# Kernel tuning notes

Measured on AMD Instinct MI355X. Metric: run time of the kernel, lower is better.

## Reference

```python
import jax, jax.numpy as jnp
import numpy as np

N_NODES = 100000
N_EDGES = 600000
HIDDEN = 128


def setup_inputs() -> dict:
    key = jax.random.key(0)
    ks = jax.random.split(key, 5)
    x = jax.random.normal(ks[0], (N_NODES, HIDDEN), dtype=jnp.float32)
    edge_index = jax.random.randint(ks[1], (2, N_EDGES), 0, N_NODES, dtype=jnp.int64)
    edge_weight = jax.random.uniform(ks[2], (N_EDGES,), dtype=jnp.float32)
    # MLP params: Linear(2*H+1 -> H), ReLU, Linear(H -> 1)
    W1 = jax.random.normal(ks[3], (2 * HIDDEN + 1, HIDDEN), dtype=jnp.float32) * (1.0 / np.sqrt(2 * HIDDEN + 1))
    b1 = jnp.zeros((HIDDEN,), dtype=jnp.float32)
    W2 = jax.random.normal(ks[4], (HIDDEN, 1), dtype=jnp.float32) * (1.0 / np.sqrt(HIDDEN))
    b2 = jnp.zeros((1,), dtype=jnp.float32)
    return {"x": x, "edge_index": edge_index, "edge_weight": edge_weight,
            "W1": W1, "b1": b1, "W2": W2, "b2": b2}


def reference(x, edge_index, edge_weight, W1, b1, W2, b2):
    num_nodes = x.shape[0]
    src = edge_index[0]
    tgt = edge_index[1]
    h_src = x[src]                      # [E, H] gather
    h_tgt = x[tgt]                      # [E, H] gather
    w = edge_weight[:, None]            # [E, 1]
    concat = jnp.concatenate([h_src, h_tgt, w], axis=-1)   # [E, 2H+1]
    hidden = jax.nn.relu(concat @ W1 + b1)                 # [E, H]
    scores = (hidden @ W2 + b2)[:, 0]                      # [E]
    # NOTE: the original _softmax_edge's max-pass uses index_put_(accumulate=True)
    # on a -inf buffer, so every touched entry stays -inf and is then replaced by 0;
    # the net effect is NO max subtraction. Faithful math: plain exp / segment_sum.
    exp_scores = jnp.exp(scores)
    sum_exp = jax.ops.segment_sum(exp_scores, tgt, num_segments=num_nodes)
    sum_exp = jnp.maximum(sum_exp, 1e-12)
    alpha = exp_scores / sum_exp[tgt]                      # [E]
    out = jax.ops.segment_sum(alpha[:, None] * h_src, tgt, num_segments=num_nodes)
    return x + out
```

## Files before the change

### kernel.cpp

```cpp
#include <hip/hip_runtime.h>
#include <hip/hip_bf16.h>

#define N_NODES 100000
#define N_EDGES 600000
#define HID 128
#define SCAN_NB 391
#define GEMM_BLOCKS 1563
#define FILL_BLOCKS 586


typedef short bf16x8 __attribute__((ext_vector_type(8)));
typedef float f32x4  __attribute__((ext_vector_type(4)));

__device__ inline unsigned short f2bf(float v) {
    __hip_bfloat16 h = __float2bfloat16(v);
    return *(unsigned short*)&h;
}
__device__ inline float2 bfpair(unsigned int u) {
    float lo = __uint_as_float(u << 16);
    float hi = __uint_as_float(u & 0xffff0000u);
    return make_float2(lo, hi);
}
__device__ inline void lds_barrier() {
    asm volatile("s_waitcnt lgkmcnt(0)" ::: "memory");
    __builtin_amdgcn_s_barrier();
}

__global__ __launch_bounds__(256) void k_prep(const float* __restrict__ W1,
                                              unsigned short* __restrict__ Bh,
                                              int* __restrict__ deg)
{
    int idx = blockIdx.x * 256 + threadIdx.x;
    if (idx < N_NODES) deg[idx] = 0;
    if (idx < 32768) {
        int n = idx & 255;
        int k = idx >> 8;
        float v = (n < HID) ? W1[k * HID + n] : W1[(HID + k) * HID + (n - HID)];
        Bh[(k >> 5) * 8192 + n * 32 + (k & 31)] = f2bf(v);
    }
}

__global__ __launch_bounds__(256) void k_count(const int* __restrict__ ei,
                                               int* __restrict__ deg)
{
    int e = blockIdx.x * blockDim.x + threadIdx.x;
    if (e < N_EDGES) atomicAdd(&deg[ei[N_EDGES + e]], 1);
}

__global__ __launch_bounds__(256) void k_rowptr(const int* __restrict__ deg,
                                                int* __restrict__ rowptr,
                                                int* __restrict__ cursor)
{
    __shared__ int s[256];
    int t = threadIdx.x;
    int b = blockIdx.x;
    int lim = b * 256;

    int acc = 0;
    for (int i = t; i < lim; i += 256) acc += deg[i];
    s[t] = acc;
    __syncthreads();
    #pragma unroll
    for (int off = 128; off > 0; off >>= 1) {
        if (t < off) s[t] += s[t + off];
        __syncthreads();
    }
    int pb = s[0];
    __syncthreads();

    int idx = lim + t;
    int v = (idx < N_NODES) ? deg[idx] : 0;
    s[t] = v;
    __syncthreads();
    #pragma unroll
    for (int off = 1; off < 256; off <<= 1) {
        int u = (t >= off) ? s[t - off] : 0;
        __syncthreads();
        s[t] += u;
        __syncthreads();
    }
    if (idx < N_NODES) {
        int r = pb + s[t] - v;
        rowptr[idx] = r;
        cursor[idx] = r;
    }
    if (idx == 0) rowptr[N_NODES] = N_EDGES;
}

__global__ __launch_bounds__(256) void k_gemm_fill(const float* __restrict__ x,
                                                   const unsigned short* __restrict__ BhG,
                                                   unsigned short* __restrict__ zbuf,
                                                   unsigned short* __restrict__ y2buf,
                                                   const int* __restrict__ ei,
                                                   const float* __restrict__ ew,
                                                   int* __restrict__ cursor,
                                                   uint2* __restrict__ eprs)
{
    __shared__ unsigned short Ah[64 * 32];

    if (blockIdx.x < FILL_BLOCKS) {
        int fb = blockIdx.x;
        for (int e = fb * 256 + threadIdx.x; e < N_EDGES; e += FILL_BLOCKS * 256) {
            int tgt = ei[N_EDGES + e];
            int pos = atomicAdd(&cursor[tgt], 1);
            eprs[pos] = make_uint2((unsigned int)ei[e], __float_as_uint(ew[e]));
        }
        return;
    }

    const int tid  = threadIdx.x;
    const int bm   = (blockIdx.x - FILL_BLOCKS) * 64;
    const int wave = tid >> 6;
    const int lane = tid & 63;
    const int q    = lane >> 4;
    const int ln   = lane & 15;

    const int rowA = tid >> 3;
    const int rowB = rowA + 32;
    const int f4   = tid & 7;
    const int gmA  = bm + rowA;
    const int gmB  = bm + rowB;
    const bool okA = gmA < N_NODES;
    const bool okB = gmB < N_NODES;
    const float* pxA = &x[(size_t)gmA * HID + f4 * 4];
    const float* pxB = &x[(size_t)gmB * HID + f4 * 4];

    f32x4 acc[4][4] = {};

    float4 vA = make_float4(0.f,0.f,0.f,0.f), vB = vA;
    float4 vAn = vA, vBn = vA;
    if (okA) vA = *(const float4*)pxA;
    if (okB) vB = *(const float4*)pxB;

    for (int ks = 0; ks < 4; ++ks) {
        const int k0 = ks * 32;
        {
            float4 v = vA;
            unsigned int ph0 = (unsigned int)f2bf(v.x) | ((unsigned int)f2bf(v.y) << 16);
            unsigned int ph1 = (unsigned int)f2bf(v.z) | ((unsigned int)f2bf(v.w) << 16);
            *(uint2*)&Ah[rowA * 32 + f4 * 4] = make_uint2(ph0, ph1);
            if (okA) *(uint2*)&zbuf[(size_t)gmA * 256 + 128 + k0 + f4 * 4] = make_uint2(ph0, ph1);
        }
        {
            float4 v = vB;
            unsigned int ph0 = (unsigned int)f2bf(v.x) | ((unsigned int)f2bf(v.y) << 16);
            unsigned int ph1 = (unsigned int)f2bf(v.z) | ((unsigned int)f2bf(v.w) << 16);
            *(uint2*)&Ah[rowB * 32 + f4 * 4] = make_uint2(ph0, ph1);
            if (okB) *(uint2*)&zbuf[(size_t)gmB * 256 + 128 + k0 + f4 * 4] = make_uint2(ph0, ph1);
        }
        lds_barrier();

        if (ks < 3) {
            vAn = okA ? *(const float4*)(pxA + (ks + 1) * 32) : make_float4(0.f,0.f,0.f,0.f);
            vBn = okB ? *(const float4*)(pxB + (ks + 1) * 32) : make_float4(0.f,0.f,0.f,0.f);
        }

        bf16x8 ah[4], bh[4];
        #pragma unroll
        for (int mt = 0; mt < 4; ++mt) {
            ah[mt] = *(const bf16x8*)&Ah[(mt * 16 + ln) * 32 + q * 8];
        }
        #pragma unroll
        for (int nt = 0; nt < 4; ++nt) {
            bh[nt] = *(const bf16x8*)&BhG[ks * 8192 + (wave * 64 + nt * 16 + ln) * 32 + q * 8];
        }
        #pragma unroll
        for (int mt = 0; mt < 4; ++mt) {
            #pragma unroll
            for (int nt = 0; nt < 4; ++nt) {
                acc[mt][nt] = __builtin_amdgcn_mfma_f32_16x16x32_bf16(bh[nt], ah[mt], acc[mt][nt], 0, 0, 0);
            }
        }
        lds_barrier();
        vA = vAn; vB = vBn;
    }

    #pragma unroll
    for (int mt = 0; mt < 4; ++mt) {
        int node = bm + mt * 16 + ln;
        if (node < N_NODES) {
            #pragma unroll
            for (int nt = 0; nt < 4; ++nt) {
                int col0 = wave * 64 + nt * 16 + q * 4;
                unsigned int lo = (unsigned int)f2bf(acc[mt][nt][0]) | ((unsigned int)f2bf(acc[mt][nt][1]) << 16);
                unsigned int hi = (unsigned int)f2bf(acc[mt][nt][2]) | ((unsigned int)f2bf(acc[mt][nt][3]) << 16);
                if (col0 < 128) *(uint2*)&zbuf[(size_t)node * 256 + col0] = make_uint2(lo, hi);
                else            *(uint2*)&y2buf[(size_t)node * 128 + (col0 - 128)] = make_uint2(lo, hi);
            }
        }
    }
}

__global__ __launch_bounds__(256) void k_fused(const unsigned int* __restrict__ zu,
                                               const unsigned int* __restrict__ y2u,
                                               const int* __restrict__ rowptr,
                                               const uint2* __restrict__ eprs,
                                               const float* __restrict__ x,
                                               const float* __restrict__ W1,
                                               const float* __restrict__ b1,
                                               const float* __restrict__ W2,
                                               const float* __restrict__ b2,
                                               float* __restrict__ out)
{
    int n = (blockIdx.x * blockDim.x + threadIdx.x) >> 6;
    int lane = threadIdx.x & 63;
    if (n >= N_NODES) return;
    int ql = lane & 15;
    int qi = lane >> 4;
    int c0 = ql * 8;

    uint4 uy2 = *(const uint4*)&y2u[(size_t)n * 64 + ql * 4];
    float2 y2a = bfpair(uy2.x), y2b = bfpair(uy2.y), y2c = bfpair(uy2.z), y2d = bfpair(uy2.w);
    float4 bv0 = *(const float4*)&b1[c0];
    float4 bv1 = *(const float4*)&b1[c0 + 4];
    float4 wr0 = *(const float4*)&W1[256 * HID + c0];
    float4 wr1 = *(const float4*)&W1[256 * HID + c0 + 4];
    float4 w20 = *(const float4*)&W2[c0];
    float4 w21 = *(const float4*)&W2[c0 + 4];
    float p0 = y2a.x + bv0.x, p1 = y2a.y + bv0.y, p2 = y2b.x + bv0.z, p3 = y2b.y + bv0.w;
    float p4 = y2c.x + bv1.x, p5 = y2c.y + bv1.y, p6 = y2d.x + bv1.z, p7 = y2d.y + bv1.w;
    float b2v = b2[0];

    int beg = rowptr[n], end = rowptr[n + 1];
    float a0 = 0.f, a1 = 0.f, a2 = 0.f, a3 = 0.f;
    float a4 = 0.f, a5 = 0.f, a6 = 0.f, a7 = 0.f;
    float denom = 0.f;

    for (int i = beg; i < end; i += 4) {
        int idx = i + qi;
        bool valid = idx < end;
        int ie = valid ? idx : (end - 1);
        uint2 ep = eprs[ie];
        size_t base = (size_t)ep.x * 128;
        float w = __uint_as_float(ep.y);
        uint4 uy = *(const uint4*)&zu[base + ql * 4];
        uint4 ux = *(const uint4*)&zu[base + 64 + ql * 4];

        float2 ya = bfpair(uy.x), yb = bfpair(uy.y), yc = bfpair(uy.z), yd = bfpair(uy.w);
        float h0 = fmaxf(fmaf(w, wr0.x, ya.x + p0), 0.f);
        float h1 = fmaxf(fmaf(w, wr0.y, ya.y + p1), 0.f);
        float h2 = fmaxf(fmaf(w, wr0.z, yb.x + p2), 0.f);
        float h3 = fmaxf(fmaf(w, wr0.w, yb.y + p3), 0.f);
        float h4 = fmaxf(fmaf(w, wr1.x, yc.x + p4), 0.f);
        float h5 = fmaxf(fmaf(w, wr1.y, yc.y + p5), 0.f);
        float h6 = fmaxf(fmaf(w, wr1.z, yd.x + p6), 0.f);
        float h7 = fmaxf(fmaf(w, wr1.w, yd.y + p7), 0.f);
        float s = ((h0 * w20.x + h1 * w20.y) + (h2 * w20.z + h3 * w20.w))
                + ((h4 * w21.x + h5 * w21.y) + (h6 * w21.z + h7 * w21.w));
        #pragma unroll
        for (int m = 1; m <= 8; m <<= 1) s += __shfl_xor(s, m, 64);
        float es = valid ? __expf(s + b2v) : 0.f;

        float2 xa = bfpair(ux.x), xb = bfpair(ux.y), xc = bfpair(ux.z), xd = bfpair(ux.w);
        a0 = fmaf(es, xa.x, a0); a1 = fmaf(es, xa.y, a1);
        a2 = fmaf(es, xb.x, a2); a3 = fmaf(es, xb.y, a3);
        a4 = fmaf(es, xc.x, a4); a5 = fmaf(es, xc.y, a5);
        a6 = fmaf(es, xd.x, a6); a7 = fmaf(es, xd.y, a7);
        denom += es;
    }

    #pragma unroll
    for (int m = 16; m <= 32; m <<= 1) {
        a0 += __shfl_xor(a0, m, 64); a1 += __shfl_xor(a1, m, 64);
        a2 += __shfl_xor(a2, m, 64); a3 += __shfl_xor(a3, m, 64);
        a4 += __shfl_xor(a4, m, 64); a5 += __shfl_xor(a5, m, 64);
        a6 += __shfl_xor(a6, m, 64); a7 += __shfl_xor(a7, m, 64);
        denom += __shfl_xor(denom, m, 64);
    }

    if (qi == 0) {
        float4 xt0 = *(const float4*)&x[(size_t)n * HID + c0];
        float4 xt1 = *(const float4*)&x[(size_t)n * HID + c0 + 4];
        float inv = 1.0f / fmaxf(denom, 1e-12f);
        float4 o0, o1;
        o0.x = xt0.x + a0 * inv; o0.y = xt0.y + a1 * inv;
        o0.z = xt0.z + a2 * inv; o0.w = xt0.w + a3 * inv;
        o1.x = xt1.x + a4 * inv; o1.y = xt1.y + a5 * inv;
        o1.z = xt1.z + a6 * inv; o1.w = xt1.w + a7 * inv;
        *(float4*)&out[(size_t)n * HID + c0]     = o0;
        *(float4*)&out[(size_t)n * HID + c0 + 4] = o1;
    }
}

extern "C" void kernel_launch(void* const* d_in, const int* in_sizes, int n_in,
                              void* d_out, int out_size, void* d_ws, size_t ws_size,
                              hipStream_t stream) {
    const float* x  = (const float*)d_in[0];
    const int*   ei = (const int*)d_in[1];
    const float* ew = (const float*)d_in[2];
    const float* W1 = (const float*)d_in[3];
    const float* b1 = (const float*)d_in[4];
    const float* W2 = (const float*)d_in[5];
    const float* b2 = (const float*)d_in[6];
    float* out = (float*)d_out;
    char* ws = (char*)d_ws;

    const size_t deg_b    = 400000;
    const size_t rowptr_b = 400016;
    const size_t cursor_b = 400000;
    const size_t eprs_b   = 4800000;
    const size_t part_b   = 1568;
    const size_t pb_b     = 1568;
    const size_t Bh_b     = 65536;

    char* p = ws;
    int* deg      = (int*)p;             p += deg_b;
    int* rowptr   = (int*)p;             p += rowptr_b;
    int* cursor   = (int*)p;             p += cursor_b;
    uint2* eprs   = (uint2*)p;           p += eprs_b;
    p += part_b;
    p += pb_b;
    unsigned short* BhG = (unsigned short*)p;  p += Bh_b;
    unsigned short* zbuf  = (unsigned short*)p;  p += (size_t)N_NODES * 256 * 2;
    unsigned short* y2buf = (unsigned short*)p;

    const int edge_blocks = (N_EDGES + 255) / 256;
    const int node_wave_blocks = (N_NODES * 64 + 255) / 256;

    hipLaunchKernelGGL(k_prep,   dim3(SCAN_NB), dim3(256), 0, stream, W1, BhG, deg);
    hipLaunchKernelGGL(k_count,  dim3(edge_blocks), dim3(256), 0, stream, ei, deg);
    hipLaunchKernelGGL(k_rowptr, dim3(SCAN_NB), dim3(256), 0, stream, deg, rowptr, cursor);
    hipLaunchKernelGGL(k_gemm_fill, dim3(GEMM_BLOCKS + FILL_BLOCKS), dim3(256), 0, stream,
                       x, BhG, zbuf, y2buf, ei, ew, cursor, eprs);
    hipLaunchKernelGGL(k_fused, dim3(node_wave_blocks), dim3(256), 0, stream,
                       (const unsigned int*)zbuf, (const unsigned int*)y2buf,
                       rowptr, eprs, x, W1, b1, W2, b2, out);
}
```

Baseline: 323.8 us.

## Stage full A tile in swizzled LDS once and reorder GEMM loops

The GEMM part of the fused gemm/fill kernel now loads each 64x128 x tile in a single pass, with wide 128-bit loads and stores, into a larger LDS buffer. It uses an XOR swizzle to avoid bank conflicts and needs only one barrier instead of two per k-step. The MFMA loop is reordered to iterate nt outermost, keeping all A fragments in registers. The block ordering is also swapped so GEMM blocks come first and fill blocks last. The cost is more LDS and register use per block, which may lower occupancy.

```diff
diff --git a/kernel.cpp b/kernel.cpp
--- a/kernel.cpp
+++ b/kernel.cpp
@@ -15,6 +15,9 @@
 __device__ inline unsigned short f2bf(float v) {
     __hip_bfloat16 h = __float2bfloat16(v);
     return *(unsigned short*)&h;
+}
+__device__ inline unsigned int pack2(float a, float b) {
+    return (unsigned int)f2bf(a) | ((unsigned int)f2bf(b) << 16);
 }
 __device__ inline float2 bfpair(unsigned int u) {
     float lo = __uint_as_float(u << 16);
@@ -96,10 +99,10 @@
                                                    int* __restrict__ cursor,
                                                    uint2* __restrict__ eprs)
 {
-    __shared__ unsigned short Ah[64 * 32];
-
-    if (blockIdx.x < FILL_BLOCKS) {
-        int fb = blockIdx.x;
+    __shared__ unsigned short Ah[64 * 128];
+
+    if (blockIdx.x >= GEMM_BLOCKS) {
+        int fb = blockIdx.x - GEMM_BLOCKS;
         for (int e = fb * 256 + threadIdx.x; e < N_EDGES; e += FILL_BLOCKS * 256) {
             int tgt = ei[N_EDGES + e];
             int pos = atomicAdd(&cursor[tgt], 1);
@@ -109,70 +112,77 @@
     }
 
     const int tid  = threadIdx.x;
-    const int bm   = (blockIdx.x - FILL_BLOCKS) * 64;
+    const int bm   = blockIdx.x * 64;
     const int wave = tid >> 6;
     const int lane = tid & 63;
     const int q    = lane >> 4;
     const int ln   = lane & 15;
 
-    const int rowA = tid >> 3;
-    const int rowB = rowA + 32;
-    const int f4   = tid & 7;
-    const int gmA  = bm + rowA;
-    const int gmB  = bm + rowB;
-    const bool okA = gmA < N_NODES;
-    const bool okB = gmB < N_NODES;
-    const float* pxA = &x[(size_t)gmA * HID + f4 * 4];
-    const float* pxB = &x[(size_t)gmB * HID + f4 * 4];
-
-    f32x4 acc[4][4] = {};
-
-    float4 vA = make_float4(0.f,0.f,0.f,0.f), vB = vA;
-    float4 vAn = vA, vBn = vA;
-    if (okA) vA = *(const float4*)pxA;
-    if (okB) vB = *(const float4*)pxB;
-
-    for (int ks = 0; ks < 4; ++ks) {
-        const int k0 = ks * 32;
-        {
-            float4 v = vA;
-            unsigned int ph0 = (unsigned int)f2bf(v.x) | ((unsigned int)f2bf(v.y) << 16);
-            unsigned int ph1 = (unsigned int)f2bf(v.z) | ((unsigned int)f2bf(v.w) << 16);
-            *(uint2*)&Ah[rowA * 32 + f4 * 4] = make_uint2(ph0, ph1);
-            if (okA) *(uint2*)&zbuf[(size_t)gmA * 256 + 128 + k0 + f4 * 4] = make_uint2(ph0, ph1);
-        }
-        {
-            float4 v = vB;
-            unsigned int ph0 = (unsigned int)f2bf(v.x) | ((unsigned int)f2bf(v.y) << 16);
-            unsigned int ph1 = (unsigned int)f2bf(v.z) | ((unsigned int)f2bf(v.w) << 16);
-            *(uint2*)&Ah[rowB * 32 + f4 * 4] = make_uint2(ph0, ph1);
-            if (okB) *(uint2*)&zbuf[(size_t)gmB * 256 + 128 + k0 + f4 * 4] = make_uint2(ph0, ph1);
-        }
-        lds_barrier();
-
-        if (ks < 3) {
-            vAn = okA ? *(const float4*)(pxA + (ks + 1) * 32) : make_float4(0.f,0.f,0.f,0.f);
-            vBn = okB ? *(const float4*)(pxB + (ks + 1) * 32) : make_float4(0.f,0.f,0.f,0.f);
-        }
-
-        bf16x8 ah[4], bh[4];
+    {
+        const int r  = tid >> 2;
+        const int c  = tid & 3;
+        const int gm = bm + r;
+        const bool ok = gm < N_NODES;
+        const float* px = &x[(size_t)gm * HID + c * 32];
+
+        float4 v0 = make_float4(0.f,0.f,0.f,0.f), v1=v0, v2=v0, v3=v0, v4=v0, v5=v0, v6=v0, v7=v0;
+        if (ok) {
+            v0 = *(const float4*)(px + 0);  v1 = *(const float4*)(px + 4);
+            v2 = *(const float4*)(px + 8);  v3 = *(const float4*)(px + 12);
+            v4 = *(const float4*)(px + 16); v5 = *(const float4*)(px + 20);
+            v6 = *(const float4*)(px + 24); v7 = *(const float4*)(px + 28);
+        }
+        uint4 ch0, ch1, ch2, ch3;
+        ch0.x = pack2(v0.x, v0.y); ch0.y = pack2(v0.z, v0.w); ch0.z = pack2(v1.x, v1.y); ch0.w = pack2(v1.z, v1.w);
+        ch1.x = pack2(v2.x, v2.y); ch1.y = pack2(v2.z, v2.w); ch1.z = pack2(v3.x, v3.y); ch1.w = pack2(v3.z, v3.w);
+        ch2.x = pack2(v4.x, v4.y); ch2.y = pack2(v4.z, v4.w); ch2.z = pack2(v5.x, v5.y); ch2.w = pack2(v5.z, v5.w);
+        ch3.x = pack2(v6.x, v6.y); ch3.y = pack2(v6.z, v6.w); ch3.z = pack2(v7.x, v7.y); ch3.w = pack2(v7.z, v7.w);
+
+        char* rowp = (char*)Ah + r * 256;
+        const int swz = (r & 7) << 4;
+        *(uint4*)(rowp + ((c * 64 +  0) ^ swz)) = ch0;
+        *(uint4*)(rowp + ((c * 64 + 16) ^ swz)) = ch1;
+        *(uint4*)(rowp + ((c * 64 + 32) ^ swz)) = ch2;
+        *(uint4*)(rowp + ((c * 64 + 48) ^ swz)) = ch3;
+
+        if (ok) {
+            unsigned short* zp = &zbuf[(size_t)gm * 256 + 128 + c * 32];
+            *(uint4*)(zp + 0)  = ch0;
+            *(uint4*)(zp + 8)  = ch1;
+            *(uint4*)(zp + 16) = ch2;
+            *(uint4*)(zp + 24) = ch3;
+        }
+    }
+    lds_barrier();
+
+    bf16x8 ah[4][4];
+    {
+        const int swzr = (ln & 7) << 4;
         #pragma unroll
         for (int mt = 0; mt < 4; ++mt) {
-            ah[mt] = *(const bf16x8*)&Ah[(mt * 16 + ln) * 32 + q * 8];
-        }
+            const char* rowp = (const char*)Ah + (mt * 16 + ln) * 256;
+            #pragma unroll
+            for (int ks = 0; ks < 4; ++ks) {
+                ah[mt][ks] = *(const bf16x8*)(rowp + ((ks * 64 + q * 16) ^ swzr));
+            }
+        }
+    }
+
+    f32x4 acc[4][4] = {};
+    #pragma unroll
+    for (int nt = 0; nt < 4; ++nt) {
+        bf16x8 bh[4];
         #pragma unroll
-        for (int nt = 0; nt < 4; ++nt) {
-            bh[nt] = *(const bf16x8*)&BhG[ks * 8192 + (wave * 64 + nt * 16 + ln) * 32 + q * 8];
+        for (int ks = 0; ks < 4; ++ks) {
+            bh[ks] = *(const bf16x8*)&BhG[ks * 8192 + (wave * 64 + nt * 16 + ln) * 32 + q * 8];
         }
         #pragma unroll
         for (int mt = 0; mt < 4; ++mt) {
             #pragma unroll
-            for (int nt = 0; nt < 4; ++nt) {
-                acc[mt][nt] = __builtin_amdgcn_mfma_f32_16x16x32_bf16(bh[nt], ah[mt], acc[mt][nt], 0, 0, 0);
+            for (int ks = 0; ks < 4; ++ks) {
+                acc[mt][nt] = __builtin_amdgcn_mfma_f32_16x16x32_bf16(bh[ks], ah[mt][ks], acc[mt][nt], 0, 0, 0);
             }
         }
-        lds_barrier();
-        vA = vAn; vB = vBn;
     }
 
     #pragma unroll
@@ -182,8 +192,8 @@
             #pragma unroll
             for (int nt = 0; nt < 4; ++nt) {
                 int col0 = wave * 64 + nt * 16 + q * 4;
-                unsigned int lo = (unsigned int)f2bf(acc[mt][nt][0]) | ((unsigned int)f2bf(acc[mt][nt][1]) << 16);
-                unsigned int hi = (unsigned int)f2bf(acc[mt][nt][2]) | ((unsigned int)f2bf(acc[mt][nt][3]) << 16);
+                unsigned int lo = pack2(acc[mt][nt][0], acc[mt][nt][1]);
+                unsigned int hi = pack2(acc[mt][nt][2], acc[mt][nt][3]);
                 if (col0 < 128) *(uint2*)&zbuf[(size_t)node * 256 + col0] = make_uint2(lo, hi);
                 else            *(uint2*)&y2buf[(size_t)node * 128 + (col0 - 128)] = make_uint2(lo, hi);
             }
```

New measurement: 316.4 us. 2.3% less time.
